# Kernel tuning notes

Measured on AMD Instinct MI355X. Metric: run time of the kernel, lower is better.

Reference implementation:

```python
import jax, jax.numpy as jnp
from jax import lax
import numpy as np

N_NODES = 50000
N_EDGES = 800000
IN_CH = 128
HEADS = 4
OUT_CH = 32
TOP_K = 8


def setup_inputs() -> dict:
    key = jax.random.key(0)
    k1, k2, k3, k4 = jax.random.split(key, 4)
    x = jax.random.normal(k1, (N_NODES, IN_CH), jnp.float32)
    edge_index = jax.random.randint(k2, (2, N_EDGES), 0, N_NODES, dtype=jnp.int32)
    scale = float(np.sqrt(2.0 / (IN_CH + HEADS * OUT_CH)))  # xavier-ish
    W = jax.random.normal(k3, (IN_CH, HEADS * OUT_CH), jnp.float32) * scale
    att = jax.random.normal(k4, (HEADS, 2 * OUT_CH), jnp.float32) * 0.1
    return {"x": x, "W": W, "att": att, "edge_index": edge_index}


def _topk_mask_1h(e_h, row, k):
    # e_h: [E'] scores for one head; keep top-k scores within each row-segment.
    E = e_h.shape[0]
    order = jnp.lexsort((-e_h, row))          # grouped by row, descending score
    srow = row[order]
    seg_start = jnp.searchsorted(srow, srow, side="left")
    pos_in_seg = jnp.arange(E, dtype=seg_start.dtype) - seg_start
    keep_sorted = pos_in_seg < k
    return jnp.zeros((E,), jnp.bool_).at[order].set(keep_sorted)


def reference(x, W, att, edge_index):
    N = x.shape[0]
    H, C = HEADS, OUT_CH
    h = (x @ W).reshape(N, H, C)              # [N,H,C]
    # add self loops
    loops = jnp.arange(N, dtype=edge_index.dtype)
    ei = jnp.concatenate([edge_index, jnp.stack([loops, loops])], axis=1)
    row, col = ei[0], ei[1]                   # [E']
    x_i = h[row]                              # [E',H,C] gather (dst)
    x_j = h[col]                              # [E',H,C] gather (src)
    a_i, a_j = att[:, :C], att[:, C:]
    e = jnp.einsum("ehc,hc->eh", x_i, a_i) + jnp.einsum("ehc,hc->eh", x_j, a_j)
    e = jax.nn.leaky_relu(e, negative_slope=0.2)  # [E',H]
    mask = jax.vmap(lambda eh: _topk_mask_1h(eh, row, TOP_K),
                    in_axes=1, out_axes=1)(e)     # [E',H] bool
    e = jnp.where(mask, e, -jnp.inf)
    # segment softmax over rows (every node has a self loop -> non-empty segment)
    seg_max = jax.ops.segment_max(e, row, num_segments=N)
    ez = jnp.exp(e - lax.stop_gradient(seg_max)[row])  # masked edges -> 0
    denom = jax.ops.segment_sum(ez, row, num_segments=N)
    alpha = ez / denom[row]                   # [E',H]
    # dropout is identity in eval mode
    out = jax.ops.segment_sum(alpha[:, :, None] * x_j, row, num_segments=N)
    out = out.reshape(N, H * C)               # concat=True
    return jax.nn.elu(out)
```

## Files before the change

### kernel.cpp

```cpp
#include <hip/hip_runtime.h>
#include <math.h>

typedef unsigned int u32;
typedef unsigned short u16;
typedef unsigned long long u64;

#define NN 50000
#define NE 800000
#define TOPK 8
#define NB 196
#define BCAP 4608
#define CURSTRIDE 16
#define PBLOCKS 391

__global__ __launch_bounds__(256) void gemm_k(const float* __restrict__ x,
                                              const float* __restrict__ W,
                                              const float* __restrict__ att,
                                              float* __restrict__ hbuf,
                                              float* __restrict__ s_i,
                                              float* __restrict__ s_j) {
    __shared__ float xst[64][132];
    __shared__ float ws[64][128];
    const int t = threadIdx.x;
    const int cx = t & 15;
    const int ry = t >> 4;
    const int rbase = blockIdx.x * 128;

    float acc[8][8];
    #pragma unroll
    for (int i = 0; i < 8; ++i)
        #pragma unroll
        for (int j = 0; j < 8; ++j) acc[i][j] = 0.f;

    for (int kk = 0; kk < 128; kk += 64) {
        if (kk) __syncthreads();
        #pragma unroll
        for (int rr = ry; rr < 128; rr += 16) {
            int gr = rbase + rr;
            float4 v = make_float4(0.f, 0.f, 0.f, 0.f);
            if (gr < NN)
                v = *reinterpret_cast<const float4*>(x + (size_t)gr * 128 + kk + cx * 4);
            xst[cx * 4 + 0][rr] = v.x;
            xst[cx * 4 + 1][rr] = v.y;
            xst[cx * 4 + 2][rr] = v.z;
            xst[cx * 4 + 3][rr] = v.w;
        }
        #pragma unroll
        for (int wk = t >> 5; wk < 64; wk += 8) {
            float4 v = *reinterpret_cast<const float4*>(W + (size_t)(kk + wk) * 128 + (t & 31) * 4);
            *reinterpret_cast<float4*>(&ws[wk][(t & 31) * 4]) = v;
        }
        __syncthreads();

        for (int k = 0; k < 64; ++k) {
            float4 xa = *reinterpret_cast<const float4*>(&xst[k][ry * 8]);
            float4 xb = *reinterpret_cast<const float4*>(&xst[k][ry * 8 + 4]);
            float4 wa = *reinterpret_cast<const float4*>(&ws[k][cx * 8]);
            float4 wb = *reinterpret_cast<const float4*>(&ws[k][cx * 8 + 4]);
            float xv[8] = {xa.x, xa.y, xa.z, xa.w, xb.x, xb.y, xb.z, xb.w};
            float wv[8] = {wa.x, wa.y, wa.z, wa.w, wb.x, wb.y, wb.z, wb.w};
            #pragma unroll
            for (int i = 0; i < 8; ++i)
                #pragma unroll
                for (int j = 0; j < 8; ++j) acc[i][j] += xv[i] * wv[j];
        }
    }

    const int head = cx >> 2;
    float aiv[8], ajv[8];
    #pragma unroll
    for (int j = 0; j < 8; ++j) {
        aiv[j] = att[head * 64 + (cx & 3) * 8 + j];
        ajv[j] = att[head * 64 + 32 + (cx & 3) * 8 + j];
    }
    #pragma unroll
    for (int i = 0; i < 8; ++i) {
        int gr = rbase + ry * 8 + i;
        float pi = 0.f, pj = 0.f;
        #pragma unroll
        for (int j = 0; j < 8; ++j) {
            pi += acc[i][j] * aiv[j];
            pj += acc[i][j] * ajv[j];
        }
        pi += __shfl_xor(pi, 1); pi += __shfl_xor(pi, 2);
        pj += __shfl_xor(pj, 1); pj += __shfl_xor(pj, 2);
        if (gr < NN) {
            float* dst = hbuf + (size_t)gr * 128 + cx * 8;
            *reinterpret_cast<float4*>(dst)     = make_float4(acc[i][0], acc[i][1], acc[i][2], acc[i][3]);
            *reinterpret_cast<float4*>(dst + 4) = make_float4(acc[i][4], acc[i][5], acc[i][6], acc[i][7]);
            if ((cx & 3) == 0) {
                s_i[(size_t)gr * 4 + head] = pi;
                s_j[(size_t)gr * 4 + head] = pj;
            }
        }
    }
}

__global__ __launch_bounds__(256) void part_k(const int* __restrict__ ei,
                                              int* __restrict__ cursor,
                                              u32* __restrict__ breg) {
    __shared__ u32 cnt[NB];
    __shared__ u32 base[NB];
    const int t = threadIdx.x;
    if (t < NB) cnt[t] = 0;
    __syncthreads();

    const int e0 = blockIdx.x * 2048 + t * 8;
    const bool ev = e0 < NE;
    int rows[8], cols[8], bk[8];
    u32 lrk[8];
    if (ev) {
        int4 ra = *reinterpret_cast<const int4*>(ei + e0);
        int4 rb = *reinterpret_cast<const int4*>(ei + e0 + 4);
        int4 ca = *reinterpret_cast<const int4*>(ei + NE + e0);
        int4 cb = *reinterpret_cast<const int4*>(ei + NE + e0 + 4);
        rows[0] = ra.x; rows[1] = ra.y; rows[2] = ra.z; rows[3] = ra.w;
        rows[4] = rb.x; rows[5] = rb.y; rows[6] = rb.z; rows[7] = rb.w;
        cols[0] = ca.x; cols[1] = ca.y; cols[2] = ca.z; cols[3] = ca.w;
        cols[4] = cb.x; cols[5] = cb.y; cols[6] = cb.z; cols[7] = cb.w;
        #pragma unroll
        for (int i = 0; i < 8; ++i) {
            bk[i] = rows[i] >> 8;
            lrk[i] = atomicAdd(&cnt[bk[i]], 1u);
        }
    }
    __syncthreads();
    if (t < NB) base[t] = (cnt[t] > 0) ? (u32)atomicAdd(cursor + t * CURSTRIDE, (int)cnt[t]) : 0u;
    __syncthreads();
    if (ev) {
        #pragma unroll
        for (int i = 0; i < 8; ++i) {
            u32 pos = base[bk[i]] + lrk[i];
            if (pos < BCAP)
                breg[(size_t)bk[i] * BCAP + pos] = ((u32)(rows[i] & 255) << 16) | (u32)cols[i];
        }
    }
}

__global__ __launch_bounds__(256) void rowsel_k(const int* __restrict__ cursor,
                                                const u32* __restrict__ breg,
                                                const float* __restrict__ s_i,
                                                const float* __restrict__ s_j,
                                                const float* __restrict__ hbuf,
                                                float* __restrict__ out) {
    __shared__ u16 lcsr[64][66];
    __shared__ u32 ldeg[64];
    __shared__ float lal[256 * 8];
    __shared__ u16  lcl[256 * 8];
    const int t = threadIdx.x;
    const int B = blockIdx.x >> 2;
    const int s = blockIdx.x & 3;
    const int rbase = B * 256 + s * 64;

    if (t < 64) ldeg[t] = 0;
    __syncthreads();

    int n = cursor[B * CURSTRIDE];
    if (n > BCAP) n = BCAP;
    const u32* reg = breg + (size_t)B * BCAP;
    for (int i = t; i < n; i += 256) {
        u32 e = reg[i];
        if ((int)(e >> 22) == s) {
            int lr = (int)((e >> 16) & 63);
            u32 rk = atomicAdd(&ldeg[lr], 1u);
            if (rk < 64) lcsr[lr][rk] = (u16)(e & 0xFFFFu);
        }
    }
    __syncthreads();

    const int lrow = t >> 2;
    const int head = t & 3;
    const int row = rbase + lrow;

    u64 kl[TOPK];
    int cl[TOPK];
    #pragma unroll
    for (int i = 0; i < TOPK; ++i) { kl[i] = 0ull; cl[i] = 0; }

    int dgr = 0;
    if (row < NN) {
        dgr = (int)ldeg[lrow];
        if (dgr > 64) dgr = 64;
        float v = s_j[(size_t)row * 4 + head];
        u32 b = __float_as_uint(v);
        u32 fk = (b & 0x80000000u) ? ~b : (b | 0x80000000u);
        kl[0] = ((u64)fk << 32) | (u32)(~(u32)(NE + row));
        cl[0] = row;
    }

    for (int j = 0; j < dgr; ++j) {
        int col = (int)lcsr[lrow][j];
        float v = s_j[(size_t)col * 4 + head];
        u32 b = __float_as_uint(v);
        u32 fk = (b & 0x80000000u) ? ~b : (b | 0x80000000u);
        u64 key = ((u64)fk << 32) | (u32)(~(u32)j);
        int cc = col;
        if (key > kl[TOPK - 1]) {
            #pragma unroll
            for (int i = 0; i < TOPK; ++i) {
                bool gt = key > kl[i];
                u64 tk = gt ? kl[i] : key;  kl[i] = gt ? key : kl[i];  key = tk;
                int tc = gt ? cl[i] : cc;   cl[i] = gt ? cc : cl[i];   cc = tc;
            }
        }
    }

    {
        float si = (row < NN) ? s_i[(size_t)row * 4 + head] : 0.f;
        u32 fk = (u32)(kl[0] >> 32);
        u32 b = (fk & 0x80000000u) ? (fk ^ 0x80000000u) : ~fk;
        float vmax = __uint_as_float(b);
        float em = si + vmax;
        float m = (em >= 0.f) ? em : 0.2f * em;
        float al[TOPK];
        float denom = 0.f;
        #pragma unroll
        for (int i = 0; i < TOPK; ++i) {
            u32 fki = (u32)(kl[i] >> 32);
            u32 bi = (fki & 0x80000000u) ? (fki ^ 0x80000000u) : ~fki;
            float v = __uint_as_float(bi);
            float e = si + v;
            e = (e >= 0.f) ? e : 0.2f * e;
            float z = (kl[i] != 0ull) ? __expf(e - m) : 0.f;
            al[i] = z;
            denom += z;
        }
        float inv = 1.f / denom;
        #pragma unroll
        for (int i = 0; i < TOPK; ++i) {
            lal[t * 8 + i] = al[i] * inv;
            lcl[t * 8 + i] = (u16)cl[i];
        }
    }
    __syncthreads();

    const int lane = t & 63;
    const int wid = t >> 6;
    const int q = lane >> 3;
    const int dq = lane & 7;
    for (int g = wid; g < 32; g += 4) {
        const int p = g * 8 + q;
        const int r = rbase + (p >> 2);
        const int hh = p & 3;
        if (r < NN) {
            const int base = p * 8;
            float av[8]; int cv[8];
            #pragma unroll
            for (int k = 0; k < 8; ++k) { av[k] = lal[base + k]; cv[k] = (int)lcl[base + k]; }
            float4 a4 = make_float4(0.f, 0.f, 0.f, 0.f);
            #pragma unroll
            for (int k = 0; k < 8; ++k) {
                const float4 hv = *reinterpret_cast<const float4*>(
                    &hbuf[(size_t)cv[k] * 128 + hh * 32 + dq * 4]);
                a4.x += av[k] * hv.x;
                a4.y += av[k] * hv.y;
                a4.z += av[k] * hv.z;
                a4.w += av[k] * hv.w;
            }
            a4.x = (a4.x > 0.f) ? a4.x : expm1f(a4.x);
            a4.y = (a4.y > 0.f) ? a4.y : expm1f(a4.y);
            a4.z = (a4.z > 0.f) ? a4.z : expm1f(a4.z);
            a4.w = (a4.w > 0.f) ? a4.w : expm1f(a4.w);
            *reinterpret_cast<float4*>(&out[(size_t)r * 128 + hh * 32 + dq * 4]) = a4;
        }
    }
}

extern "C" void kernel_launch(void* const* d_in, const int* in_sizes, int n_in,
                              void* d_out, int out_size, void* d_ws, size_t ws_size,
                              hipStream_t stream) {
    const float* x   = (const float*)d_in[0];
    const float* W   = (const float*)d_in[1];
    const float* att = (const float*)d_in[2];
    const int*   ei  = (const int*)d_in[3];
    float* out = (float*)d_out;

    u32* breg    = (u32*)d_ws;
    float* hbuf  = (float*)(breg + (size_t)NB * BCAP);
    float* s_i   = hbuf + 6400000;
    float* s_j   = s_i + 200000;
    int* cursor  = (int*)(s_j + 200000);

    hipMemsetAsync(cursor, 0, NB * CURSTRIDE * sizeof(int), stream);
    gemm_k<<<(NN + 127) / 128, 256, 0, stream>>>(x, W, att, hbuf, s_i, s_j);
    part_k<<<PBLOCKS, 256, 0, stream>>>(ei, cursor, breg);
    rowsel_k<<<NB * 4, 256, 0, stream>>>(cursor, breg, s_i, s_j, hbuf, out);
}
```

Before: 173.5 us.

## Fuse edge bucket partitioning into the GEMM kernel

Folds the edge partitioning pass into the GEMM kernel, since both launch 391 blocks. Each block loads its edge indices up front, does the shared-memory bucket counting after the first k-tile sync, and does the global cursor atomics after the second. It scatters edges into the bucket regions after the GEMM epilogue. This removes one kernel launch and overlaps the scattered edge traffic with GEMM compute, at the cost of extra registers and shared memory in the GEMM kernel, which could reduce occupancy.

```diff
diff --git a/kernel.cpp b/kernel.cpp
--- a/kernel.cpp
+++ b/kernel.cpp
@@ -11,20 +11,41 @@
 #define NB 196
 #define BCAP 4608
 #define CURSTRIDE 16
-#define PBLOCKS 391
+#define GTILES 391
 
 __global__ __launch_bounds__(256) void gemm_k(const float* __restrict__ x,
                                               const float* __restrict__ W,
                                               const float* __restrict__ att,
+                                              const int* __restrict__ ei,
                                               float* __restrict__ hbuf,
                                               float* __restrict__ s_i,
-                                              float* __restrict__ s_j) {
+                                              float* __restrict__ s_j,
+                                              int* __restrict__ cursor,
+                                              u32* __restrict__ breg) {
     __shared__ float xst[64][132];
     __shared__ float ws[64][128];
+    __shared__ u32 cnt[NB];
+    __shared__ u32 base[NB];
     const int t = threadIdx.x;
     const int cx = t & 15;
     const int ry = t >> 4;
     const int rbase = blockIdx.x * 128;
+
+    const int e0 = blockIdx.x * 2048 + t * 8;
+    const bool ev = e0 < NE;
+    int4 ra = make_int4(0,0,0,0), rb = make_int4(0,0,0,0);
+    int4 ca = make_int4(0,0,0,0), cb = make_int4(0,0,0,0);
+    if (ev) {
+        ra = *reinterpret_cast<const int4*>(ei + e0);
+        rb = *reinterpret_cast<const int4*>(ei + e0 + 4);
+        ca = *reinterpret_cast<const int4*>(ei + NE + e0);
+        cb = *reinterpret_cast<const int4*>(ei + NE + e0 + 4);
+    }
+    if (t < NB) cnt[t] = 0;
+
+    int bk[8];
+    u32 lrk[8] = {0,0,0,0,0,0,0,0};
+    u32 myBase = 0;
 
     float acc[8][8];
     #pragma unroll
@@ -52,6 +73,20 @@
         }
         __syncthreads();
 
+        if (kk == 0) {
+            if (ev) {
+                int rows[8] = {ra.x, ra.y, ra.z, ra.w, rb.x, rb.y, rb.z, rb.w};
+                #pragma unroll
+                for (int i = 0; i < 8; ++i) {
+                    bk[i] = rows[i] >> 8;
+                    lrk[i] = atomicAdd(&cnt[bk[i]], 1u);
+                }
+            }
+        } else {
+            if (t < NB && cnt[t] > 0)
+                myBase = (u32)atomicAdd(cursor + t * CURSTRIDE, (int)cnt[t]);
+        }
+
         for (int k = 0; k < 64; ++k) {
             float4 xa = *reinterpret_cast<const float4*>(&xst[k][ry * 8]);
             float4 xb = *reinterpret_cast<const float4*>(&xst[k][ry * 8 + 4]);
@@ -94,40 +129,12 @@
             }
         }
     }
-}
-
-__global__ __launch_bounds__(256) void part_k(const int* __restrict__ ei,
-                                              int* __restrict__ cursor,
-                                              u32* __restrict__ breg) {
-    __shared__ u32 cnt[NB];
-    __shared__ u32 base[NB];
-    const int t = threadIdx.x;
-    if (t < NB) cnt[t] = 0;
-    __syncthreads();
-
-    const int e0 = blockIdx.x * 2048 + t * 8;
-    const bool ev = e0 < NE;
-    int rows[8], cols[8], bk[8];
-    u32 lrk[8];
+
+    if (t < NB) base[t] = myBase;
+    __syncthreads();
     if (ev) {
-        int4 ra = *reinterpret_cast<const int4*>(ei + e0);
-        int4 rb = *reinterpret_cast<const int4*>(ei + e0 + 4);
-        int4 ca = *reinterpret_cast<const int4*>(ei + NE + e0);
-        int4 cb = *reinterpret_cast<const int4*>(ei + NE + e0 + 4);
-        rows[0] = ra.x; rows[1] = ra.y; rows[2] = ra.z; rows[3] = ra.w;
-        rows[4] = rb.x; rows[5] = rb.y; rows[6] = rb.z; rows[7] = rb.w;
-        cols[0] = ca.x; cols[1] = ca.y; cols[2] = ca.z; cols[3] = ca.w;
-        cols[4] = cb.x; cols[5] = cb.y; cols[6] = cb.z; cols[7] = cb.w;
-        #pragma unroll
-        for (int i = 0; i < 8; ++i) {
-            bk[i] = rows[i] >> 8;
-            lrk[i] = atomicAdd(&cnt[bk[i]], 1u);
-        }
-    }
-    __syncthreads();
-    if (t < NB) base[t] = (cnt[t] > 0) ? (u32)atomicAdd(cursor + t * CURSTRIDE, (int)cnt[t]) : 0u;
-    __syncthreads();
-    if (ev) {
+        int rows[8] = {ra.x, ra.y, ra.z, ra.w, rb.x, rb.y, rb.z, rb.w};
+        int cols[8] = {ca.x, ca.y, ca.z, ca.w, cb.x, cb.y, cb.z, cb.w};
         #pragma unroll
         for (int i = 0; i < 8; ++i) {
             u32 pos = base[bk[i]] + lrk[i];
@@ -282,7 +289,6 @@
     int* cursor  = (int*)(s_j + 200000);
 
     hipMemsetAsync(cursor, 0, NB * CURSTRIDE * sizeof(int), stream);
-    gemm_k<<<(NN + 127) / 128, 256, 0, stream>>>(x, W, att, hbuf, s_i, s_j);
-    part_k<<<PBLOCKS, 256, 0, stream>>>(ei, cursor, breg);
+    gemm_k<<<GTILES, 256, 0, stream>>>(x, W, att, ei, hbuf, s_i, s_j, cursor, breg);
     rowsel_k<<<NB * 4, 256, 0, stream>>>(cursor, breg, s_i, s_j, hbuf, out);
 }
```

New measurement: 164.0 us. 5.5% less time.
